# Kernel tuning notes

Measured on AMD Instinct MI355X. Metric: run time of the kernel, lower is better.

Reference implementation:

```python
import jax, jax.numpy as jnp
import numpy as np

BATCH_SIZE = 4096
DIM = 512
TEMPERATURE = 0.5
NUM_CLASSES = 100
EPS = 1e-8  # torch CosineSimilarity eps


def setup_inputs() -> dict:
    key = jax.random.key(0)
    k1, k2, k3 = jax.random.split(key, 3)
    z = jax.random.normal(k1, (BATCH_SIZE, DIM), dtype=jnp.float32)
    z_adv = jax.random.normal(k2, (BATCH_SIZE, DIM), dtype=jnp.float32)
    labels = jax.random.randint(k3, (BATCH_SIZE,), 0, NUM_CLASSES, dtype=jnp.int64)
    return {"z": z, "z_adv": z_adv, "labels": labels}


def _normalize(x):
    # torch.nn.CosineSimilarity clamps norm at eps
    n = jnp.sqrt(jnp.sum(x * x, axis=-1, keepdims=True))
    return x / jnp.maximum(n, EPS)


def reference(z, z_adv, labels):
    N = z.shape[0]
    zn = _normalize(z)            # [N, D]
    zan = _normalize(z_adv)       # [N, D]
    # per-sample clean-vs-adv cosine similarity
    sim_adv = jnp.sum(zn * zan, axis=1) / TEMPERATURE      # [N]
    sim_adv_e = jnp.exp(sim_adv)
    # pairwise cosine similarity via normalize + matmul (same math as
    # the broadcasted CosineSimilarity(dim=2) in the original)
    sim = jnp.einsum('nd,md->nm', zn, zn) / TEMPERATURE     # [N, N]
    # mask: same label, off-diagonal
    same = labels[None, :] == labels[:, None]
    mask = same & ~jnp.eye(N, dtype=bool)
    intra = jnp.sum(jnp.exp(sim) * mask.astype(sim.dtype), axis=1)  # [N]
    loss = -jnp.log(sim_adv_e / (sim_adv_e + intra))
    return jnp.sum(loss) / N
```

## Files before the change

### kernel.cpp

```cpp
#include <hip/hip_runtime.h>
#include <math.h>

#define N      4096
#define DIM    512
#define NCLS   100
#define INV_T  2.0f
#define EPSN   1e-8f
#define CAP    96
#define NTMAX  (CAP / 16)
#define FRAG_SHORTS (NTMAX * 16 * 64 * 8)
#define NTHR   1024
#define NWAVE  16

#define OFF_INTRA (FRAG_SHORTS * 2)
#define OFF_SADV  (OFF_INTRA + CAP * 4)
#define OFF_RNRM  (OFF_SADV  + CAP * 4)
#define OFF_SLOT  (OFF_RNRM  + CAP * 4)
#define OFF_WRED  (OFF_SLOT  + CAP * 4)
#define OFF_CNT   (OFF_WRED  + NWAVE * 4)
#define SMEM_BYTES (OFF_CNT + 4)

typedef __attribute__((ext_vector_type(8))) short short8;
typedef __attribute__((ext_vector_type(4))) float float4v;

__device__ __forceinline__ float dot8(const float4& a0, const float4& a1,
                                      const float4& b0, const float4& b1) {
    float p = a0.x * b0.x;
    p = fmaf(a0.y, b0.y, p); p = fmaf(a0.z, b0.z, p); p = fmaf(a0.w, b0.w, p);
    p = fmaf(a1.x, b1.x, p); p = fmaf(a1.y, b1.y, p);
    p = fmaf(a1.z, b1.z, p); p = fmaf(a1.w, b1.w, p);
    return p;
}

__device__ __forceinline__ short f2bf(float x) {
    unsigned u = __float_as_uint(x);
    unsigned r = (u + 0x7FFFu + ((u >> 16) & 1u)) >> 16;
    return (short)r;
}

__global__ __launch_bounds__(NTHR, 4)
void ial_fused_kernel(const float* __restrict__ z,
                      const float* __restrict__ za,
                      const int*   __restrict__ labels,
                      float* __restrict__ out) {
    extern __shared__ char smem[];
    short* frag  = (short*)smem;
    float* intra = (float*)(smem + OFF_INTRA);
    float* sadv  = (float*)(smem + OFF_SADV);
    float* rnrm  = (float*)(smem + OFF_RNRM);
    int*   slot  = (int*)  (smem + OFF_SLOT);
    float* wred  = (float*)(smem + OFF_WRED);
    int*   cnt   = (int*)  (smem + OFF_CNT);

    const int c    = blockIdx.x;
    const int tid  = threadIdx.x;
    const int wave = tid >> 6, lane = tid & 63;

    if (tid == 0) *cnt = 0;
    __syncthreads();
    {
        int4 l4 = ((const int4*)labels)[tid];
        const int b = tid * 4;
        if (l4.x == c) { int p = atomicAdd(cnt, 1); if (p < CAP) slot[p] = b; }
        if (l4.y == c) { int p = atomicAdd(cnt, 1); if (p < CAP) slot[p] = b + 1; }
        if (l4.z == c) { int p = atomicAdd(cnt, 1); if (p < CAP) slot[p] = b + 2; }
        if (l4.w == c) { int p = atomicAdd(cnt, 1); if (p < CAP) slot[p] = b + 3; }
    }
    __syncthreads();
    int m = *cnt; if (m > CAP) m = CAP;
    const int nt = (m + 15) >> 4;

    const int kt_w = lane >> 2, q_w = lane & 3;
    for (int s = wave; s < nt * 16; s += NWAVE) {
        const int tile = s >> 4, col = s & 15;
        short8 v;
        if (s < m) {
            const int j = slot[s];
            const float4* zr = (const float4*)(z  + (size_t)j * DIM);
            const float4* ar = (const float4*)(za + (size_t)j * DIM);
            float4 f0 = zr[lane * 2], f1 = zr[lane * 2 + 1];
            float4 g0 = ar[lane * 2], g1 = ar[lane * 2 + 1];
            v[0] = f2bf(f0.x); v[1] = f2bf(f0.y); v[2] = f2bf(f0.z); v[3] = f2bf(f0.w);
            v[4] = f2bf(f1.x); v[5] = f2bf(f1.y); v[6] = f2bf(f1.z); v[7] = f2bf(f1.w);
            float zz  = dot8(f0, f1, f0, f1);
            float aa  = dot8(g0, g1, g0, g1);
            float zad = dot8(f0, f1, g0, g1);
            #pragma unroll
            for (int off = 32; off >= 1; off >>= 1) {
                zz  += __shfl_xor(zz,  off);
                aa  += __shfl_xor(aa,  off);
                zad += __shfl_xor(zad, off);
            }
            if (lane == 0) {
                const float nz = fmaxf(sqrtf(zz), EPSN);
                const float na = fmaxf(sqrtf(aa), EPSN);
                rnrm[s] = 1.0f / nz;
                sadv[s] = zad / (nz * na) * INV_T;
            }
        } else {
            v = (short8)0;
            if (lane == 0) { rnrm[s] = 0.f; sadv[s] = 0.f; }
        }
        *(short8*)(frag + (((size_t)(tile * 16 + kt_w) * 64 + q_w * 16 + col) * 8)) = v;
    }
    __syncthreads();

    const int q = lane >> 4, col = lane & 15;
    for (int ti = wave; ti < nt; ti += NWAVE) {
        short8 a[16];
        #pragma unroll
        for (int kt = 0; kt < 16; ++kt)
            a[kt] = *(const short8*)(frag + (((ti * 16 + kt) * 64 + lane) * 8));
        const int irow = ti * 16 + q * 4;
        const float rni0 = rnrm[irow + 0] * INV_T;
        const float rni1 = rnrm[irow + 1] * INV_T;
        const float rni2 = rnrm[irow + 2] * INV_T;
        const float rni3 = rnrm[irow + 3] * INV_T;
        float racc0 = 0.f, racc1 = 0.f, racc2 = 0.f, racc3 = 0.f;
        for (int tj = 0; tj < nt; ++tj) {
            float4v acc = {0.f, 0.f, 0.f, 0.f};
            #pragma unroll
            for (int kt = 0; kt < 16; ++kt) {
                short8 b = *(const short8*)(frag + (((tj * 16 + kt) * 64 + lane) * 8));
                acc = __builtin_amdgcn_mfma_f32_16x16x32_bf16(a[kt], b, acc, 0, 0, 0);
            }
            const int jslot = tj * 16 + col;
            const bool jok = (jslot < m);
            const float rnj = rnrm[jslot];
            racc0 += (jok && (irow + 0) != jslot) ? __expf(acc[0] * rni0 * rnj) : 0.f;
            racc1 += (jok && (irow + 1) != jslot) ? __expf(acc[1] * rni1 * rnj) : 0.f;
            racc2 += (jok && (irow + 2) != jslot) ? __expf(acc[2] * rni2 * rnj) : 0.f;
            racc3 += (jok && (irow + 3) != jslot) ? __expf(acc[3] * rni3 * rnj) : 0.f;
        }
        #pragma unroll
        for (int off = 1; off < 16; off <<= 1) {
            racc0 += __shfl_xor(racc0, off);
            racc1 += __shfl_xor(racc1, off);
            racc2 += __shfl_xor(racc2, off);
            racc3 += __shfl_xor(racc3, off);
        }
        if (col == 0) {
            intra[irow + 0] = racc0;
            intra[irow + 1] = racc1;
            intra[irow + 2] = racc2;
            intra[irow + 3] = racc3;
        }
    }
    __syncthreads();

    float lsum = 0.f;
    for (int s = tid; s < m; s += NTHR) {
        const float sa = sadv[s];
        lsum += logf(__expf(sa) + intra[s]) - sa;
    }
    #pragma unroll
    for (int off = 32; off >= 1; off >>= 1) lsum += __shfl_xor(lsum, off);
    if (lane == 0) wred[wave] = lsum;
    __syncthreads();
    if (tid == 0) {
        float t = 0.f;
        #pragma unroll
        for (int w = 0; w < NWAVE; ++w) t += wred[w];
        atomicAdd(out, t * (1.0f / (float)N));
    }
}

extern "C" void kernel_launch(void* const* d_in, const int* in_sizes, int n_in,
                              void* d_out, int out_size, void* d_ws, size_t ws_size,
                              hipStream_t stream) {
    const float* z      = (const float*)d_in[0];
    const float* z_adv  = (const float*)d_in[1];
    const int*   labels = (const int*)d_in[2];

    static int attr_done = 0;
    if (!attr_done) {
        hipFuncSetAttribute((const void*)ial_fused_kernel,
                            hipFuncAttributeMaxDynamicSharedMemorySize, SMEM_BYTES);
        attr_done = 1;
    }

    hipMemsetAsync(d_out, 0, sizeof(float), stream);
    ial_fused_kernel<<<NCLS, NTHR, SMEM_BYTES, stream>>>(z, z_adv, labels,
                                                         (float*)d_out);
}
```

Measured before the change: 75.69 us.

## Split Gram tile pairs across waves and batch two row loads per wave

The row-tile loop becomes a loop over (ti,tj) tile pairs spread across all 16 waves, with per-row sums combined through shared-memory atomicAdd into a zero-initialised intra array. The goal is to use more waves than the few row tiles (nt is about 3 here), which left most waves idle. The staging loop now has each wave issue global loads for two slots before converting them, so more memory requests are in flight at once. The cost is extra LDS atomics and reloading the A fragments for every pair.

Result: no change. 75.41 us (-0.4%).

```diff
diff --git a/kernel.cpp b/kernel.cpp
--- a/kernel.cpp
+++ b/kernel.cpp
@@ -36,6 +36,38 @@
     unsigned u = __float_as_uint(x);
     unsigned r = (u + 0x7FFFu + ((u >> 16) & 1u)) >> 16;
     return (short)r;
+}
+
+__device__ __forceinline__ void stage_slot(short* frag, float* rnrm, float* sadv,
+                                           int s, int m, int lane,
+                                           const float4& f0, const float4& f1,
+                                           const float4& g0, const float4& g1) {
+    const int tile = s >> 4, col = s & 15;
+    const int kt_w = lane >> 2, q_w = lane & 3;
+    short8 v;
+    if (s < m) {
+        v[0] = f2bf(f0.x); v[1] = f2bf(f0.y); v[2] = f2bf(f0.z); v[3] = f2bf(f0.w);
+        v[4] = f2bf(f1.x); v[5] = f2bf(f1.y); v[6] = f2bf(f1.z); v[7] = f2bf(f1.w);
+        float zz  = dot8(f0, f1, f0, f1);
+        float aa  = dot8(g0, g1, g0, g1);
+        float zad = dot8(f0, f1, g0, g1);
+        #pragma unroll
+        for (int off = 32; off >= 1; off >>= 1) {
+            zz  += __shfl_xor(zz,  off);
+            aa  += __shfl_xor(aa,  off);
+            zad += __shfl_xor(zad, off);
+        }
+        if (lane == 0) {
+            const float nz = fmaxf(sqrtf(zz), EPSN);
+            const float na = fmaxf(sqrtf(aa), EPSN);
+            rnrm[s] = 1.0f / nz;
+            sadv[s] = zad / (nz * na) * INV_T;
+        }
+    } else {
+        v = (short8)0;
+        if (lane == 0) { rnrm[s] = 0.f; sadv[s] = 0.f; }
+    }
+    *(short8*)(frag + (((size_t)(tile * 16 + kt_w) * 64 + q_w * 16 + col) * 8)) = v;
 }
 
 __global__ __launch_bounds__(NTHR, 4)
@@ -57,6 +89,7 @@
     const int wave = tid >> 6, lane = tid & 63;
 
     if (tid == 0) *cnt = 0;
+    if (tid < CAP) intra[tid] = 0.f;
     __syncthreads();
     {
         int4 l4 = ((const int4*)labels)[tid];
@@ -69,81 +102,66 @@
     __syncthreads();
     int m = *cnt; if (m > CAP) m = CAP;
     const int nt = (m + 15) >> 4;
-
-    const int kt_w = lane >> 2, q_w = lane & 3;
-    for (int s = wave; s < nt * 16; s += NWAVE) {
-        const int tile = s >> 4, col = s & 15;
-        short8 v;
+    const int ntot = nt * 16;
+
+    for (int s = wave; s < ntot; s += 2 * NWAVE) {
+        const int sB = s + NWAVE;
+        const bool hasB = (sB < ntot);
+        float4 fA0{}, fA1{}, gA0{}, gA1{}, fB0{}, fB1{}, gB0{}, gB1{};
         if (s < m) {
             const int j = slot[s];
             const float4* zr = (const float4*)(z  + (size_t)j * DIM);
             const float4* ar = (const float4*)(za + (size_t)j * DIM);
-            float4 f0 = zr[lane * 2], f1 = zr[lane * 2 + 1];
-            float4 g0 = ar[lane * 2], g1 = ar[lane * 2 + 1];
-            v[0] = f2bf(f0.x); v[1] = f2bf(f0.y); v[2] = f2bf(f0.z); v[3] = f2bf(f0.w);
-            v[4] = f2bf(f1.x); v[5] = f2bf(f1.y); v[6] = f2bf(f1.z); v[7] = f2bf(f1.w);
-            float zz  = dot8(f0, f1, f0, f1);
-            float aa  = dot8(g0, g1, g0, g1);
-            float zad = dot8(f0, f1, g0, g1);
-            #pragma unroll
-            for (int off = 32; off >= 1; off >>= 1) {
-                zz  += __shfl_xor(zz,  off);
-                aa  += __shfl_xor(aa,  off);
-                zad += __shfl_xor(zad, off);
-            }
-            if (lane == 0) {
-                const float nz = fmaxf(sqrtf(zz), EPSN);
-                const float na = fmaxf(sqrtf(aa), EPSN);
-                rnrm[s] = 1.0f / nz;
-                sadv[s] = zad / (nz * na) * INV_T;
-            }
-        } else {
-            v = (short8)0;
-            if (lane == 0) { rnrm[s] = 0.f; sadv[s] = 0.f; }
-        }
-        *(short8*)(frag + (((size_t)(tile * 16 + kt_w) * 64 + q_w * 16 + col) * 8)) = v;
+            fA0 = zr[lane * 2]; fA1 = zr[lane * 2 + 1];
+            gA0 = ar[lane * 2]; gA1 = ar[lane * 2 + 1];
+        }
+        if (hasB && sB < m) {
+            const int j = slot[sB];
+            const float4* zr = (const float4*)(z  + (size_t)j * DIM);
+            const float4* ar = (const float4*)(za + (size_t)j * DIM);
+            fB0 = zr[lane * 2]; fB1 = zr[lane * 2 + 1];
+            gB0 = ar[lane * 2]; gB1 = ar[lane * 2 + 1];
+        }
+        stage_slot(frag, rnrm, sadv, s, m, lane, fA0, fA1, gA0, gA1);
+        if (hasB) stage_slot(frag, rnrm, sadv, sB, m, lane, fB0, fB1, gB0, gB1);
     }
     __syncthreads();
 
     const int q = lane >> 4, col = lane & 15;
-    for (int ti = wave; ti < nt; ti += NWAVE) {
-        short8 a[16];
-        #pragma unroll
-        for (int kt = 0; kt < 16; ++kt)
-            a[kt] = *(const short8*)(frag + (((ti * 16 + kt) * 64 + lane) * 8));
-        const int irow = ti * 16 + q * 4;
+    const int npairs = nt * nt;
+    for (int p = wave; p < npairs; p += NWAVE) {
+        const int ti = p / nt, tj = p - ti * nt;
+        float4v acc = {0.f, 0.f, 0.f, 0.f};
+        #pragma unroll
+        for (int kt = 0; kt < 16; ++kt) {
+            short8 a = *(const short8*)(frag + (((ti * 16 + kt) * 64 + lane) * 8));
+            short8 b = *(const short8*)(frag + (((tj * 16 + kt) * 64 + lane) * 8));
+            acc = __builtin_amdgcn_mfma_f32_16x16x32_bf16(a, b, acc, 0, 0, 0);
+        }
+        const int irow  = ti * 16 + q * 4;
+        const int jslot = tj * 16 + col;
+        const bool jok  = (jslot < m);
+        const float rnj = rnrm[jslot];
         const float rni0 = rnrm[irow + 0] * INV_T;
         const float rni1 = rnrm[irow + 1] * INV_T;
         const float rni2 = rnrm[irow + 2] * INV_T;
         const float rni3 = rnrm[irow + 3] * INV_T;
-        float racc0 = 0.f, racc1 = 0.f, racc2 = 0.f, racc3 = 0.f;
-        for (int tj = 0; tj < nt; ++tj) {
-            float4v acc = {0.f, 0.f, 0.f, 0.f};
-            #pragma unroll
-            for (int kt = 0; kt < 16; ++kt) {
-                short8 b = *(const short8*)(frag + (((tj * 16 + kt) * 64 + lane) * 8));
-                acc = __builtin_amdgcn_mfma_f32_16x16x32_bf16(a[kt], b, acc, 0, 0, 0);
-            }
-            const int jslot = tj * 16 + col;
-            const bool jok = (jslot < m);
-            const float rnj = rnrm[jslot];
-            racc0 += (jok && (irow + 0) != jslot) ? __expf(acc[0] * rni0 * rnj) : 0.f;
-            racc1 += (jok && (irow + 1) != jslot) ? __expf(acc[1] * rni1 * rnj) : 0.f;
-            racc2 += (jok && (irow + 2) != jslot) ? __expf(acc[2] * rni2 * rnj) : 0.f;
-            racc3 += (jok && (irow + 3) != jslot) ? __expf(acc[3] * rni3 * rnj) : 0.f;
-        }
+        float e0 = (jok && (irow + 0) != jslot) ? __expf(acc[0] * rni0 * rnj) : 0.f;
+        float e1 = (jok && (irow + 1) != jslot) ? __expf(acc[1] * rni1 * rnj) : 0.f;
+        float e2 = (jok && (irow + 2) != jslot) ? __expf(acc[2] * rni2 * rnj) : 0.f;
+        float e3 = (jok && (irow + 3) != jslot) ? __expf(acc[3] * rni3 * rnj) : 0.f;
         #pragma unroll
         for (int off = 1; off < 16; off <<= 1) {
-            racc0 += __shfl_xor(racc0, off);
-            racc1 += __shfl_xor(racc1, off);
-            racc2 += __shfl_xor(racc2, off);
-            racc3 += __shfl_xor(racc3, off);
+            e0 += __shfl_xor(e0, off);
+            e1 += __shfl_xor(e1, off);
+            e2 += __shfl_xor(e2, off);
+            e3 += __shfl_xor(e3, off);
         }
         if (col == 0) {
-            intra[irow + 0] = racc0;
-            intra[irow + 1] = racc1;
-            intra[irow + 2] = racc2;
-            intra[irow + 3] = racc3;
+            atomicAdd(&intra[irow + 0], e0);
+            atomicAdd(&intra[irow + 1], e1);
+            atomicAdd(&intra[irow + 2], e2);
+            atomicAdd(&intra[irow + 3], e3);
         }
     }
     __syncthreads();
```
